# Performance work log

Measured on AMD Instinct MI355X. Metric: run time of the kernel, lower is better.

The kernel has to match this reference:

```python
import jax, jax.numpy as jnp
import numpy as np

H = 80  # HIDDEN_SIZE


def _cell(x, h, c, w_ih, w_hh, b_ih, b_hh):
    # torch LSTMCell: gates ordered i, f, g, o
    g = x @ w_ih.T + b_ih + h @ w_hh.T + b_hh  # (B, 4H)
    i, f, gg, o = jnp.split(g, 4, axis=-1)
    c = jax.nn.sigmoid(f) * c + jax.nn.sigmoid(i) * jnp.tanh(gg)
    h = jax.nn.sigmoid(o) * jnp.tanh(c)
    return h, c


def setup_inputs() -> dict:
    key = jax.random.key(0)
    ks = jax.random.split(key, 24)
    B, T = 4096, 512
    s = 1.0 / np.sqrt(H)
    u = lambda k, shape: jax.random.uniform(k, shape, jnp.float32, -s, s)
    inp = {"input": jax.random.normal(ks[0], (B, T), jnp.float32)}
    in_sizes = [1, H, H, H]
    for l in range(4):
        inp[f"w_ih{l+1}"] = u(ks[1 + 4 * l], (4 * H, in_sizes[l]))
        inp[f"w_hh{l+1}"] = u(ks[2 + 4 * l], (4 * H, H))
        inp[f"b_ih{l+1}"] = u(ks[3 + 4 * l], (4 * H,))
        inp[f"b_hh{l+1}"] = u(ks[4 + 4 * l], (4 * H,))
    inp["w_lin"] = u(ks[17], (1, H))
    inp["b_lin"] = u(ks[18], (1,))
    inp["future"] = 0
    return inp


def reference(input, w_ih1, w_hh1, b_ih1, b_hh1, w_ih2, w_hh2, b_ih2, b_hh2,
              w_ih3, w_hh3, b_ih3, b_hh3, w_ih4, w_hh4, b_ih4, b_hh4,
              w_lin, b_lin, future):
    B = input.shape[0]
    z = jnp.zeros((B, H), input.dtype)

    def run_step(carry, x_t):
        h1, c1, h2, c2, h3, c3, h4, c4 = carry
        h1, c1 = _cell(x_t, h1, c1, w_ih1, w_hh1, b_ih1, b_hh1)
        h2, c2 = _cell(h1, h2, c2, w_ih2, w_hh2, b_ih2, b_hh2)
        h3, c3 = _cell(h2, h3, c3, w_ih3, w_hh3, b_ih3, b_hh3)
        h4, c4 = _cell(h3, h4, c4, w_ih4, w_hh4, b_ih4, b_hh4)
        out = h2 @ w_lin.T + b_lin  # NOTE: original uses layer-2 hidden
        return (h1, c1, h2, c2, h3, c3, h4, c4), out

    xs = input.T[:, :, None]  # (T, B, 1)
    carry, outs = jax.lax.scan(run_step, (z,) * 8, xs)
    outputs = outs[..., 0].T  # (B, T)

    if future > 0:
        out = outs[-1]  # (B, 1)
        fut = []
        for _ in range(future):
            carry, out = run_step(carry, out)
            fut.append(out[:, 0])
        outputs = jnp.concatenate([outputs, jnp.stack(fut, axis=1)], axis=1)
    return outputs
```

## Files before the change

### kernel.cpp

```cpp
#include <hip/hip_runtime.h>

typedef float v4f __attribute__((ext_vector_type(4)));
typedef _Float16 h8 __attribute__((ext_vector_type(8)));

#define TT 512
#define BB 4096
#define BT 16
#define NTH 256
#define ARS 328
#define NHB 36
#define HBB 20480
#define STREAM_BYTES (NHB * HBB)

__global__ void prep_pack(const float* __restrict__ whh1,
                          const float* __restrict__ wih2, const float* __restrict__ whh2,
                          const float* __restrict__ wih3, const float* __restrict__ whh3,
                          const float* __restrict__ wih4, const float* __restrict__ whh4,
                          _Float16* __restrict__ stream)
{
  int e = blockIdx.x * blockDim.x + threadIdx.x;
  if (e >= NHB * (HBB / 2)) return;
  int hb = e / (HBB / 2);
  int r  = e - hb * (HBB / 2);
  int T  = r >> 9;
  int r2 = r & 511;
  int L  = r2 >> 3;
  int j  = r2 & 7;
  int ks = hb >> 1;
  int is_lo = hb & 1;
  int l = (ks < 3) ? 0 : (ks < 8) ? 1 : (ks < 13) ? 2 : 3;
  int s = ks - ((l == 0) ? 0 : (l == 1) ? 3 : (l == 2) ? 8 : 13);
  int n = 16 * T + (L & 15);
  int k = 32 * s + ((L >> 4) << 3) + j;
  float w;
  if (l == 0) {
    w = (k < 80) ? whh1[n * 80 + k] : 0.f;
  } else {
    const float* wih = (l == 1) ? wih2 : (l == 2) ? wih3 : wih4;
    const float* whh = (l == 1) ? whh2 : (l == 2) ? whh3 : whh4;
    w = (k < 80) ? wih[n * 80 + k] : whh[n * 80 + (k - 80)];
  }
  _Float16 hi = (_Float16)w;
  _Float16 v = is_lo ? (_Float16)((w - (float)hi) * 4096.f) : hi;
  stream[e] = v;
}

__device__ __forceinline__ float sigm(float x) {
  return __builtin_amdgcn_rcpf(1.f + __expf(-x));
}
__device__ __forceinline__ float tanh_fast(float x) {
  return 1.f - 2.f * __builtin_amdgcn_rcpf(1.f + __expf(2.f * x));
}
__device__ __forceinline__ void bar() {
  asm volatile("s_waitcnt lgkmcnt(0)" ::: "memory");
  __builtin_amdgcn_s_barrier();
  asm volatile("" ::: "memory");
}

__global__ void __launch_bounds__(NTH, 1)
lstm_main(const float* __restrict__ input,
          const _Float16* __restrict__ stream,
          const float* __restrict__ bih1, const float* __restrict__ bhh1,
          const float* __restrict__ bih2, const float* __restrict__ bhh2,
          const float* __restrict__ bih3, const float* __restrict__ bhh3,
          const float* __restrict__ bih4, const float* __restrict__ bhh4,
          const float* __restrict__ wih1, const float* __restrict__ wlin,
          const float* __restrict__ blin, float* __restrict__ out)
{
  __shared__ __align__(16) float s_gates[320 * 20];
  __shared__ __align__(16) _Float16 s_Ahi[16 * ARS];
  __shared__ __align__(16) _Float16 s_Alo[16 * ARS];
  __shared__ __align__(16) float s_h2[80 * 16];
  __shared__ __align__(16) float s_bias[4 * 320];
  __shared__ __align__(16) float s_wih1[320];
  __shared__ __align__(16) float s_wlin[80];
  __shared__ __align__(16) float s_xb[16];

  const int tid  = threadIdx.x;
  const int lane = tid & 63;
  const int wv   = tid >> 6;
  const int b0   = blockIdx.x * BT;
  const int m15  = lane & 15;
  const int quad = lane >> 4;
  const int mb   = quad * 4;
  const int jb   = tid & 15;
  const int j0   = tid >> 4;

  for (int i = tid; i < 320; i += NTH) {
    s_bias[i]       = bih1[i] + bhh1[i];
    s_bias[320 + i] = bih2[i] + bhh2[i];
    s_bias[640 + i] = bih3[i] + bhh3[i];
    s_bias[960 + i] = bih4[i] + bhh4[i];
    s_wih1[i] = wih1[i];
  }
  for (int i = tid; i < 80; i += NTH) s_wlin[i] = wlin[i];
  for (int i = tid; i < 16 * ARS / 2; i += NTH) {
    ((unsigned*)s_Ahi)[i] = 0u;
    ((unsigned*)s_Alo)[i] = 0u;
  }
  if (tid < 16) s_xb[tid] = input[(b0 + tid) * TT];
  const float blinv = blin[0];

  v4f bf[4][5];
  const char* sbase = (const char*)stream + wv * 5120 + lane * 16;
#define ISSUE(H) do { const char* p_ = sbase + (H) * HBB;      \
    bf[(H) & 3][0] = *(const v4f*)(p_);                        \
    bf[(H) & 3][1] = *(const v4f*)(p_ + 1024);                 \
    bf[(H) & 3][2] = *(const v4f*)(p_ + 2048);                 \
    bf[(H) & 3][3] = *(const v4f*)(p_ + 3072);                 \
    bf[(H) & 3][4] = *(const v4f*)(p_ + 4096); } while (0)

  ISSUE(0); ISSUE(1); ISSUE(2);

  float creg[4][5];
#pragma unroll
  for (int l = 0; l < 4; ++l)
#pragma unroll
    for (int i = 0; i < 5; ++i) creg[l][i] = 0.f;

  float xreg = 0.f;
  bar();

  for (int t = 0; t < TT; ++t) {
#pragma unroll
    for (int l = 0; l < 4; ++l) {
      const int NSL = (l == 0) ? 3 : 5;
      const int KBL = (l == 0) ? 0 : (l == 1) ? 3 : (l == 2) ? 8 : 13;
      const int CBL = (l == 0) ? 0 : 80 * (l - 1);

      v4f acch[5], accl[5];
#pragma unroll
      for (int tl = 0; tl < 5; ++tl) {
        const int n = 16 * (5 * wv + tl) + m15;
        const float b = s_bias[l * 320 + n];
        v4f a;
        if (l == 0) {
          const float wi = s_wih1[n];
#pragma unroll
          for (int r = 0; r < 4; ++r) a[r] = b + s_xb[mb + r] * wi;
        } else {
#pragma unroll
          for (int r = 0; r < 4; ++r) a[r] = b;
        }
        acch[tl] = a;
        accl[tl] = (v4f){0.f, 0.f, 0.f, 0.f};
      }

      const int ab0 = m15 * ARS + CBL + quad * 8;
      h8 ahi = *(const h8*)&s_Ahi[ab0];
      h8 alo = *(const h8*)&s_Alo[ab0];
#pragma unroll
      for (int s = 0; s < NSL; ++s) {
        const int q = 2 * (KBL + s);
        ISSUE((q + 3) % NHB);
        h8 anh, anl;
        if (s + 1 < NSL) {
          anh = *(const h8*)&s_Ahi[ab0 + 32 * (s + 1)];
          anl = *(const h8*)&s_Alo[ab0 + 32 * (s + 1)];
        }
#pragma unroll
        for (int tl = 0; tl < 5; ++tl)
          acch[tl] = __builtin_amdgcn_mfma_f32_16x16x32_f16(
              ahi, __builtin_bit_cast(h8, bf[q & 3][tl]), acch[tl], 0, 0, 0);
#pragma unroll
        for (int tl = 0; tl < 5; ++tl)
          accl[tl] = __builtin_amdgcn_mfma_f32_16x16x32_f16(
              alo, __builtin_bit_cast(h8, bf[q & 3][tl]), accl[tl], 0, 0, 0);
        ISSUE((q + 4) % NHB);
#pragma unroll
        for (int tl = 0; tl < 5; ++tl)
          accl[tl] = __builtin_amdgcn_mfma_f32_16x16x32_f16(
              ahi, __builtin_bit_cast(h8, bf[(q + 1) & 3][tl]), accl[tl], 0, 0, 0);
        if (s + 1 < NSL) { ahi = anh; alo = anl; }
      }

#pragma unroll
      for (int tl = 0; tl < 5; ++tl) {
        const int n = 16 * (5 * wv + tl) + m15;
        v4f o = acch[tl] + accl[tl] * 0.000244140625f;
        *(v4f*)&s_gates[n * 20 + mb] = o;
      }
      bar();

#pragma unroll
      for (int i = 0; i < 5; ++i) {
        const int j = j0 + 16 * i;
        const float gi = s_gates[j * 20 + jb];
        const float gf = s_gates[(80 + j) * 20 + jb];
        const float gg = s_gates[(160 + j) * 20 + jb];
        const float go = s_gates[(240 + j) * 20 + jb];
        const float cn = sigm(gf) * creg[l][i] + sigm(gi) * tanh_fast(gg);
        creg[l][i] = cn;
        const float h = sigm(go) * tanh_fast(cn);
        const _Float16 hh = (_Float16)h;
        s_Ahi[jb * ARS + 80 * l + j] = hh;
        s_Alo[jb * ARS + 80 * l + j] = (_Float16)((h - (float)hh) * 4096.f);
        if (l == 1) s_h2[j * 16 + jb] = h;
      }
      if (l == 0 && tid < 16)
        xreg = input[(b0 + tid) * TT + ((t + 1 < TT) ? (t + 1) : t)];
      if (l == 3 && tid < 16) s_xb[tid] = xreg;
      bar();

      if (l == 1 && tid < 64) {
        const int ob = tid >> 2, kp = tid & 3;
        float p = 0.f;
#pragma unroll
        for (int k = 0; k < 20; ++k)
          p = fmaf(s_h2[(kp * 20 + k) * 16 + ob], s_wlin[kp * 20 + k], p);
        p += __shfl_xor(p, 1);
        p += __shfl_xor(p, 2);
        if (kp == 0) out[(b0 + ob) * TT + t] = p + blinv;
      }
    }
  }
#undef ISSUE
}

extern "C" void kernel_launch(void* const* d_in, const int* in_sizes, int n_in,
                              void* d_out, int out_size, void* d_ws, size_t ws_size,
                              hipStream_t stream) {
  const float* input = (const float*)d_in[0];
  const float* wih1 = (const float*)d_in[1];
  const float* whh1 = (const float*)d_in[2];
  const float* bih1 = (const float*)d_in[3];
  const float* bhh1 = (const float*)d_in[4];
  const float* wih2 = (const float*)d_in[5];
  const float* whh2 = (const float*)d_in[6];
  const float* bih2 = (const float*)d_in[7];
  const float* bhh2 = (const float*)d_in[8];
  const float* wih3 = (const float*)d_in[9];
  const float* whh3 = (const float*)d_in[10];
  const float* bih3 = (const float*)d_in[11];
  const float* bhh3 = (const float*)d_in[12];
  const float* wih4 = (const float*)d_in[13];
  const float* whh4 = (const float*)d_in[14];
  const float* bih4 = (const float*)d_in[15];
  const float* bhh4 = (const float*)d_in[16];
  const float* wlin = (const float*)d_in[17];
  const float* blin = (const float*)d_in[18];
  _Float16* ws = (_Float16*)d_ws;
  float* out = (float*)d_out;

  hipLaunchKernelGGL(prep_pack, dim3((NHB * (HBB / 2) + 255) / 256), dim3(256), 0,
                     stream, whh1, wih2, whh2, wih3, whh3, wih4, whh4, ws);

  hipLaunchKernelGGL(lstm_main, dim3(BB / BT), dim3(NTH), 0, stream,
                     input, ws,
                     bih1, bhh1, bih2, bhh2, bih3, bhh3, bih4, bhh4,
                     wih1, wlin, blin, out);
}
```

Baseline: 17.63 ms.

## Stream weights through an LDS ring via global_load_lds instead of registers

Replaces the register-held weight prefetch buffers with a 4-slot per-wave LDS ring filled by direct global-to-LDS loads. MFMA operands are then read from LDS, with vmcnt waits controlling how far ahead the loads run. The aim is to cut VGPR pressure and let the weight stream overlap with compute. In exchange it adds LDS traffic and more dynamic shared memory (about 140KB), and relies on the per-wave vmcnt accounting being correct.

```diff
diff --git a/kernel.cpp b/kernel.cpp
--- a/kernel.cpp
+++ b/kernel.cpp
@@ -10,7 +10,17 @@
 #define ARS 328
 #define NHB 36
 #define HBB 20480
-#define STREAM_BYTES (NHB * HBB)
+
+#define WRING_OFF 0
+#define GATES_OFF 81920
+#define AHI_OFF  107520
+#define ALO_OFF  118016
+#define H2_OFF   128512
+#define BIAS_OFF 133632
+#define WIH1_OFF 138752
+#define WLIN_OFF 140032
+#define XB_OFF   140352
+#define LDS_BYTES 140416
 
 __global__ void prep_pack(const float* __restrict__ whh1,
                           const float* __restrict__ wih2, const float* __restrict__ whh2,
@@ -57,6 +67,21 @@
   asm volatile("" ::: "memory");
 }
 
+typedef __attribute__((address_space(1))) void gvoid_t;
+typedef __attribute__((address_space(3))) void svoid_t;
+
+__device__ __forceinline__ void stage(const char* stream, char* wring,
+                                      int wv, int lane, int hq) {
+  const int hb = hq % NHB;
+  const int slot = hq & 3;
+  const char* src = stream + hb * HBB + wv * 5120 + lane * 16;
+  char* dst = wring + wv * 20480 + slot * 5120;
+#pragma unroll
+  for (int i = 0; i < 5; ++i)
+    __builtin_amdgcn_global_load_lds((gvoid_t*)(src + i * 1024),
+                                     (svoid_t*)(dst + i * 1024), 16, 0, 0);
+}
+
 __global__ void __launch_bounds__(NTH, 1)
 lstm_main(const float* __restrict__ input,
           const _Float16* __restrict__ stream,
@@ -67,14 +92,16 @@
           const float* __restrict__ wih1, const float* __restrict__ wlin,
           const float* __restrict__ blin, float* __restrict__ out)
 {
-  __shared__ __align__(16) float s_gates[320 * 20];
-  __shared__ __align__(16) _Float16 s_Ahi[16 * ARS];
-  __shared__ __align__(16) _Float16 s_Alo[16 * ARS];
-  __shared__ __align__(16) float s_h2[80 * 16];
-  __shared__ __align__(16) float s_bias[4 * 320];
-  __shared__ __align__(16) float s_wih1[320];
-  __shared__ __align__(16) float s_wlin[80];
-  __shared__ __align__(16) float s_xb[16];
+  extern __shared__ __align__(16) char smraw[];
+  char*      wring   = smraw + WRING_OFF;
+  float*     s_gates = (float*)(smraw + GATES_OFF);
+  _Float16*  s_Ahi   = (_Float16*)(smraw + AHI_OFF);
+  _Float16*  s_Alo   = (_Float16*)(smraw + ALO_OFF);
+  float*     s_h2    = (float*)(smraw + H2_OFF);
+  float*     s_bias  = (float*)(smraw + BIAS_OFF);
+  float*     s_wih1  = (float*)(smraw + WIH1_OFF);
+  float*     s_wlin  = (float*)(smraw + WLIN_OFF);
+  float*     s_xb    = (float*)(smraw + XB_OFF);
 
   const int tid  = threadIdx.x;
   const int lane = tid & 63;
@@ -101,16 +128,14 @@
   if (tid < 16) s_xb[tid] = input[(b0 + tid) * TT];
   const float blinv = blin[0];
 
-  v4f bf[4][5];
-  const char* sbase = (const char*)stream + wv * 5120 + lane * 16;
-#define ISSUE(H) do { const char* p_ = sbase + (H) * HBB;      \
-    bf[(H) & 3][0] = *(const v4f*)(p_);                        \
-    bf[(H) & 3][1] = *(const v4f*)(p_ + 1024);                 \
-    bf[(H) & 3][2] = *(const v4f*)(p_ + 2048);                 \
-    bf[(H) & 3][3] = *(const v4f*)(p_ + 3072);                 \
-    bf[(H) & 3][4] = *(const v4f*)(p_ + 4096); } while (0)
-
-  ISSUE(0); ISSUE(1); ISSUE(2);
+  const char* st8 = (const char*)stream;
+  const char* wbase = wring + wv * 20480;
+  const int lane16 = lane * 16;
+
+  stage(st8, wring, wv, lane, 0);
+  stage(st8, wring, wv, lane, 1);
+  stage(st8, wring, wv, lane, 2);
+  stage(st8, wring, wv, lane, 3);
 
   float creg[4][5];
 #pragma unroll
@@ -152,25 +177,32 @@
 #pragma unroll
       for (int s = 0; s < NSL; ++s) {
         const int q = 2 * (KBL + s);
-        ISSUE((q + 3) % NHB);
+        asm volatile("s_waitcnt vmcnt(10)" ::: "memory");
+        h8 bhi[5], blo[5];
+#pragma unroll
+        for (int tl = 0; tl < 5; ++tl)
+          bhi[tl] = *(const h8*)(wbase + (q & 3) * 5120 + tl * 1024 + lane16);
+#pragma unroll
+        for (int tl = 0; tl < 5; ++tl)
+          blo[tl] = *(const h8*)(wbase + ((q + 1) & 3) * 5120 + tl * 1024 + lane16);
         h8 anh, anl;
         if (s + 1 < NSL) {
           anh = *(const h8*)&s_Ahi[ab0 + 32 * (s + 1)];
           anl = *(const h8*)&s_Alo[ab0 + 32 * (s + 1)];
         }
-#pragma unroll
-        for (int tl = 0; tl < 5; ++tl)
-          acch[tl] = __builtin_amdgcn_mfma_f32_16x16x32_f16(
-              ahi, __builtin_bit_cast(h8, bf[q & 3][tl]), acch[tl], 0, 0, 0);
-#pragma unroll
-        for (int tl = 0; tl < 5; ++tl)
-          accl[tl] = __builtin_amdgcn_mfma_f32_16x16x32_f16(
-              alo, __builtin_bit_cast(h8, bf[q & 3][tl]), accl[tl], 0, 0, 0);
-        ISSUE((q + 4) % NHB);
-#pragma unroll
-        for (int tl = 0; tl < 5; ++tl)
-          accl[tl] = __builtin_amdgcn_mfma_f32_16x16x32_f16(
-              ahi, __builtin_bit_cast(h8, bf[(q + 1) & 3][tl]), accl[tl], 0, 0, 0);
+        asm volatile("s_waitcnt lgkmcnt(0)" ::: "memory");
+        __builtin_amdgcn_sched_barrier(0);
+        stage(st8, wring, wv, lane, q + 4);
+        stage(st8, wring, wv, lane, q + 5);
+#pragma unroll
+        for (int tl = 0; tl < 5; ++tl)
+          acch[tl] = __builtin_amdgcn_mfma_f32_16x16x32_f16(ahi, bhi[tl], acch[tl], 0, 0, 0);
+#pragma unroll
+        for (int tl = 0; tl < 5; ++tl)
+          accl[tl] = __builtin_amdgcn_mfma_f32_16x16x32_f16(alo, bhi[tl], accl[tl], 0, 0, 0);
+#pragma unroll
+        for (int tl = 0; tl < 5; ++tl)
+          accl[tl] = __builtin_amdgcn_mfma_f32_16x16x32_f16(ahi, blo[tl], accl[tl], 0, 0, 0);
         if (s + 1 < NSL) { ahi = anh; alo = anl; }
       }
 
@@ -214,7 +246,6 @@
       }
     }
   }
-#undef ISSUE
 }
 
 extern "C" void kernel_launch(void* const* d_in, const int* in_sizes, int n_in,
@@ -245,7 +276,9 @@
   hipLaunchKernelGGL(prep_pack, dim3((NHB * (HBB / 2) + 255) / 256), dim3(256), 0,
                      stream, whh1, wih2, whh2, wih3, whh3, wih4, whh4, ws);
 
-  hipLaunchKernelGGL(lstm_main, dim3(BB / BT), dim3(NTH), 0, stream,
+  hipFuncSetAttribute(reinterpret_cast<const void*>(lstm_main),
+                      hipFuncAttributeMaxDynamicSharedMemorySize, LDS_BYTES);
+  hipLaunchKernelGGL(lstm_main, dim3(BB / BT), dim3(NTH), LDS_BYTES, stream,
                      input, ws,
                      bih1, bhh1, bih2, bhh2, bih3, bhh3, bih4, bhh4,
                      wih1, wlin, blin, out);
```

Result: no change. 17.69 ms (+0.3%).
